# Kernel optimization log

Hardware: AMD Instinct MI355X
Metric: run time of the kernel (lower is better)

Reference implementation:

```python
import jax, jax.numpy as jnp
import numpy as np

NUM_HEADS = 16
HIDDEN = 1024
ATTN_DIM = 64            # per-head q/k dim
HEAD_OUT = 64            # per-head v dim
OUT_DIM = 1024
BATCH, SEQ = 2, 2048


def setup_inputs() -> dict:
    key = jax.random.key(0)
    ks = jax.random.split(key, 9)
    s_in = 1.0 / np.sqrt(HIDDEN)
    s_o = 1.0 / np.sqrt(NUM_HEADS * HEAD_OUT)
    return {
        "x": jax.random.normal(ks[0], (BATCH, SEQ, HIDDEN), dtype=jnp.float32),
        # Linear weights stored [in, out] so y = x @ W + b
        "Wq": jax.random.uniform(ks[1], (HIDDEN, NUM_HEADS * ATTN_DIM), jnp.float32, -s_in, s_in),
        "bq": jax.random.uniform(ks[2], (NUM_HEADS * ATTN_DIM,), jnp.float32, -s_in, s_in),
        "Wk": jax.random.uniform(ks[3], (HIDDEN, NUM_HEADS * ATTN_DIM), jnp.float32, -s_in, s_in),
        "bk": jax.random.uniform(ks[4], (NUM_HEADS * ATTN_DIM,), jnp.float32, -s_in, s_in),
        "Wv": jax.random.uniform(ks[5], (HIDDEN, NUM_HEADS * HEAD_OUT), jnp.float32, -s_in, s_in),
        "bv": jax.random.uniform(ks[6], (HIDDEN, NUM_HEADS * HEAD_OUT)[1:], jnp.float32, -s_in, s_in),
        "Wo": jax.random.uniform(ks[7], (NUM_HEADS * HEAD_OUT, OUT_DIM), jnp.float32, -s_o, s_o),
        "bo": jax.random.uniform(ks[8], (OUT_DIM,), jnp.float32, -s_o, s_o),
    }


def _split_heads(y, h):
    b, s, _ = y.shape
    return y.reshape(b, s, h, -1).transpose(0, 2, 1, 3)  # [b, h, s, d]


def reference(x, Wq, bq, Wk, bk, Wv, bv, Wo, bo):
    h = NUM_HEADS
    q = _split_heads(x @ Wq + bq, h)                    # [b,h,s,dq]
    k = _split_heads(x @ Wk + bk, h)                    # [b,h,s,dq]
    v = _split_heads(x @ Wv + bv, h)                    # [b,h,s,dv]
    scale = 1.0 / jnp.sqrt(jnp.float32(ATTN_DIM))
    # pattern[b,h,i,j] = key_i . query_j  (i=key index, j=query index)
    pattern = jnp.einsum('bhid,bhjd->bhij', k, q) * scale
    # softmax over key axis (dim=-2), matching t.softmax(..., dim=-2)
    prob = jax.nn.softmax(pattern, axis=-2)             # [b,h,key,query]
    # out[b,h,s,d] = sum_i prob[b,h,i,s] * v[b,h,i,d]
    out = jnp.einsum('bhis,bhid->bhsd', prob, v)        # [b,h,s,dv]
    b, _, s, dv = out.shape
    concat = out.transpose(0, 2, 1, 3).reshape(b, s, h * dv)
    return concat @ Wo + bo
```

## Files before the change

kernel.cpp:

```cpp
#include <hip/hip_runtime.h>
#include <cstdint>
#include <cstddef>

using f16   = _Float16;
using f16x4 = __attribute__((ext_vector_type(4))) _Float16;
using f16x8 = __attribute__((ext_vector_type(8))) _Float16;
using f32x4 = __attribute__((ext_vector_type(4))) float;

__device__ __forceinline__ f32x4 mfma16(f16x8 a, f16x8 b, f32x4 c) {
  return __builtin_amdgcn_mfma_f32_16x16x32_f16(a, b, c, 0, 0, 0);
}

__device__ __forceinline__ void gld16(const f16* g, f16* l) {
  __builtin_amdgcn_global_load_lds(
      (__attribute__((address_space(1))) void*)g,
      (__attribute__((address_space(3))) void*)l, 16, 0, 0);
}

constexpr int BATCH = 2, SEQL = 2048, HID = 1024, NH = 16, DH = 64;
constexpr int TOK = BATCH * SEQL;
constexpr int NQKV = 3 * HID;

__global__ __launch_bounds__(256) void k_convert_x(const float* __restrict__ x,
                                                   f16* __restrict__ xh) {
  int i = (blockIdx.x * 256 + threadIdx.x) * 4;
  float4 v = *(const float4*)(x + i);
  f16x4 o = { (f16)v.x, (f16)v.y, (f16)v.z, (f16)v.w };
  *(f16x4*)(xh + i) = o;
}

__global__ __launch_bounds__(256) void k_transpose(const float* __restrict__ Wq,
                                                   const float* __restrict__ Wk,
                                                   const float* __restrict__ Wv,
                                                   const float* __restrict__ Wo,
                                                   f16* __restrict__ WT,
                                                   f16* __restrict__ WoT) {
  __shared__ float tile[32][33];
  int mat = blockIdx.z;
  const float* W = (mat == 0) ? Wq : (mat == 1) ? Wk : (mat == 2) ? Wv : Wo;
  int in0 = blockIdx.x * 32, out0 = blockIdx.y * 32;
  int c = threadIdx.x & 31, r8 = threadIdx.x >> 5;
#pragma unroll
  for (int i = 0; i < 4; i++) {
    int r = r8 + i * 8;
    tile[r][c] = W[(size_t)(in0 + r) * HID + out0 + c];
  }
  __syncthreads();
#pragma unroll
  for (int i = 0; i < 4; i++) {
    int r = r8 + i * 8;
    f16 v = (f16)tile[c][r];
    if (mat == 3) WoT[(size_t)(out0 + r) * HID + in0 + c] = v;
    else          WT[(size_t)(mat * HID + out0 + r) * HID + in0 + c] = v;
  }
}

__global__ __launch_bounds__(256, 2) void k_gemm_qkv(
    const f16* __restrict__ xh, const f16* __restrict__ WT,
    const float* __restrict__ bq, const float* __restrict__ bk,
    const float* __restrict__ bv,
    f16* __restrict__ Qh, f16* __restrict__ Kh, f16* __restrict__ Vp) {
  constexpr int K = HID;
  int m0 = blockIdx.x * 128, n0 = blockIdx.y * 128;
  int tid = threadIdx.x;
  int w = tid >> 6, lane = tid & 63, lr = lane & 15, lq = lane >> 4;
  int wm = w >> 1, wn = w & 1;
  __shared__ f16 Ash[128 * 32];
  __shared__ f16 Bsh[128 * 32];
  f32x4 acc[4][4];
#pragma unroll
  for (int i = 0; i < 4; i++)
#pragma unroll
    for (int j = 0; j < 4; j++) acc[i][j] = (f32x4){0.f, 0.f, 0.f, 0.f};

  int row0 = tid >> 2, seg0 = tid & 3;
  int row1 = (256 + tid) >> 2;
  const f16* Ag0 = xh + (size_t)(m0 + row0) * K + seg0 * 8;
  const f16* Ag1 = xh + (size_t)(m0 + row1) * K + seg0 * 8;
  const f16* Bg0 = WT + (size_t)(n0 + row0) * K + seg0 * 8;
  const f16* Bg1 = WT + (size_t)(n0 + row1) * K + seg0 * 8;

  for (int k0 = 0; k0 < K; k0 += 32) {
    __syncthreads();
    gld16(Ag0 + k0, Ash + tid * 8);
    gld16(Ag1 + k0, Ash + (256 + tid) * 8);
    gld16(Bg0 + k0, Bsh + tid * 8);
    gld16(Bg1 + k0, Bsh + (256 + tid) * 8);
    __syncthreads();
    f16x8 af[4], bfr[4];
#pragma unroll
    for (int mt = 0; mt < 4; mt++)
      af[mt] = *(const f16x8*)(Ash + (wm * 64 + mt * 16 + lr) * 32 + lq * 8);
#pragma unroll
    for (int nt = 0; nt < 4; nt++)
      bfr[nt] = *(const f16x8*)(Bsh + (wn * 64 + nt * 16 + lr) * 32 + lq * 8);
#pragma unroll
    for (int mt = 0; mt < 4; mt++)
#pragma unroll
      for (int nt = 0; nt < 4; nt++)
        acc[mt][nt] = mfma16(af[mt], bfr[nt], acc[mt][nt]);
  }

#pragma unroll
  for (int nt = 0; nt < 4; nt++) {
    int o = n0 + wn * 64 + nt * 16 + lr;
    int sec = o >> 10, o1 = o & 1023, hh = o1 >> 6, dd = o1 & 63;
    float bias = (sec == 0) ? bq[o1] : (sec == 1) ? bk[o1] : bv[o1];
#pragma unroll
    for (int mt = 0; mt < 4; mt++) {
      int t0 = m0 + wm * 64 + mt * 16 + lq * 4;
      int b = t0 >> 11, s0 = t0 & (SEQL - 1);
      size_t bh = (size_t)(b * NH + hh);
      if (sec == 2) {
        f16x4 pv = { (f16)(acc[mt][nt][0] + bias), (f16)(acc[mt][nt][1] + bias),
                     (f16)(acc[mt][nt][2] + bias), (f16)(acc[mt][nt][3] + bias) };
        int pb = (s0 & ~31) | ((s0 & 12) << 1) | ((s0 >> 2) & 4);
        *(f16x4*)(Vp + (bh * DH + dd) * SEQL + pb) = pv;
      } else {
        f16* dst = (sec == 0) ? Qh : Kh;
#pragma unroll
        for (int r = 0; r < 4; r++)
          dst[(bh * SEQL + s0 + r) * DH + dd] = (f16)(acc[mt][nt][r] + bias);
      }
    }
  }
}

__global__ __launch_bounds__(512, 4) void k_attn(const f16* __restrict__ Qh,
                                                 const f16* __restrict__ Kh,
                                                 const f16* __restrict__ Vp,
                                                 f16* __restrict__ Ao) {
  int bh = blockIdx.x;
  int qblk = blockIdx.y;
  int b = bh >> 4, h = bh & 15;
  int tid = threadIdx.x;
  int w = tid >> 6;
  int g = w >> 2;
  int wq = w & 3;
  int lane = tid & 63, lr = lane & 15, lq = lane >> 4;

  __shared__ f16 sh[8 * 64 * 64];

  f16x8 qf[2][2];
#pragma unroll
  for (int qt = 0; qt < 2; qt++) {
    const f16* Qbase =
        Qh + ((size_t)bh * SEQL + qblk * 128 + wq * 32 + qt * 16 + lr) * DH;
#pragma unroll
    for (int ks = 0; ks < 2; ks++) {
      qf[qt][ks] = *(const f16x8*)(Qbase + ks * 32 + lq * 8);
      qf[qt][ks] = qf[qt][ks] * (f16)0.18033688f;
    }
  }

  f32x4 O[2][4];
#pragma unroll
  for (int qt = 0; qt < 2; qt++)
#pragma unroll
    for (int dt = 0; dt < 4; dt++) O[qt][dt] = (f32x4){0.f, 0.f, 0.f, 0.f};
  float lsum[2] = {0.f, 0.f};

  int sg = w >> 2, kv = (w >> 1) & 1, half = w & 1;
  int srow8 = lane >> 3;
  int scol = ((lane & 7) ^ srow8) * 8;
  const f16* sgl;
  size_t pstride, kbstride;
  if (kv == 0) {
    sgl = Kh + ((size_t)bh * SEQL + sg * 1024 + half * 32 + srow8) * DH + scol;
    pstride = (size_t)8 * DH;
    kbstride = (size_t)64 * DH;
  } else {
    sgl = Vp + ((size_t)bh * DH + half * 32 + srow8) * SEQL + sg * 1024 + scol;
    pstride = (size_t)8 * SEQL;
    kbstride = (size_t)64;
  }
  f16* sdst0 = sh + (sg * 4 + kv) * 4096 + half * 2048 + lane * 8;
  f16* sdst1 = sdst0 + 8192;

  int swz = lr & 7;
  int c0 = ((0 * 4 + lq) ^ swz) * 8;
  int c1 = ((1 * 4 + lq) ^ swz) * 8;

#pragma unroll
  for (int p8 = 0; p8 < 4; p8++) gld16(sgl + p8 * pstride, sdst0 + p8 * 512);

  for (int kb = 0; kb < 16; kb++) {
    __syncthreads();
    if (kb < 15) {
      const f16* src = sgl + (size_t)(kb + 1) * kbstride;
      f16* sd = ((kb + 1) & 1) ? sdst1 : sdst0;
#pragma unroll
      for (int p8 = 0; p8 < 4; p8++) gld16(src + p8 * pstride, sd + p8 * 512);
    }

    const f16* Kp = sh + (g * 4 + (kb & 1) * 2) * 4096;
    const f16* Vq = Kp + 4096;

    f32x4 sacc[2][4];
#pragma unroll
    for (int qt = 0; qt < 2; qt++)
#pragma unroll
      for (int kt = 0; kt < 4; kt++) sacc[qt][kt] = (f32x4){0.f, 0.f, 0.f, 0.f};
    __builtin_amdgcn_s_setprio(1);
#pragma unroll
    for (int ks = 0; ks < 2; ks++) {
      int kc = ks ? c1 : c0;
#pragma unroll
      for (int kt = 0; kt < 4; kt++) {
        f16x8 kf = *(const f16x8*)(Kp + (kt * 16 + lr) * 64 + kc);
        sacc[0][kt] = mfma16(kf, qf[0][ks], sacc[0][kt]);
        sacc[1][kt] = mfma16(kf, qf[1][ks], sacc[1][kt]);
      }
    }
    __builtin_amdgcn_s_setprio(0);

    f16x8 pf[2][2];
#pragma unroll
    for (int qt = 0; qt < 2; qt++) {
      float part = 0.f;
#pragma unroll
      for (int kt = 0; kt < 4; kt++) {
        float p0 = __builtin_amdgcn_exp2f(sacc[qt][kt][0]);
        float p1 = __builtin_amdgcn_exp2f(sacc[qt][kt][1]);
        float p2 = __builtin_amdgcn_exp2f(sacc[qt][kt][2]);
        float p3 = __builtin_amdgcn_exp2f(sacc[qt][kt][3]);
        part += (p0 + p1) + (p2 + p3);
        int s = kt >> 1, off = (kt & 1) * 4;
        pf[qt][s][off + 0] = (f16)p0; pf[qt][s][off + 1] = (f16)p1;
        pf[qt][s][off + 2] = (f16)p2; pf[qt][s][off + 3] = (f16)p3;
      }
      lsum[qt] += part;
    }

    __builtin_amdgcn_s_setprio(1);
#pragma unroll
    for (int s = 0; s < 2; s++) {
      int vc = s ? c1 : c0;
#pragma unroll
      for (int dt = 0; dt < 4; dt++) {
        f16x8 vf = *(const f16x8*)(Vq + (dt * 16 + lr) * 64 + vc);
        O[0][dt] = mfma16(vf, pf[0][s], O[0][dt]);
        O[1][dt] = mfma16(vf, pf[1][s], O[1][dt]);
      }
    }
    __builtin_amdgcn_s_setprio(0);
  }

  __syncthreads();
  float* part = (float*)sh;
  float* plsum = part + 128 * 64;
  if (g == 1) {
#pragma unroll
    for (int qt = 0; qt < 2; qt++) {
      int ql = wq * 32 + qt * 16 + lr;
#pragma unroll
      for (int dt = 0; dt < 4; dt++) {
        int slot = (dt * 4 + lq) ^ lr;
        *(f32x4*)(part + ql * 64 + slot * 4) = O[qt][dt];
      }
      plsum[ql * 4 + lq] = lsum[qt];
    }
  }
  __syncthreads();
  if (g == 0) {
#pragma unroll
    for (int qt = 0; qt < 2; qt++) {
      int ql = wq * 32 + qt * 16 + lr;
      float ls = lsum[qt] + plsum[ql * 4 + lq];
      float l1 = ls + __shfl_xor(ls, 16);
      float ltot = l1 + __shfl_xor(l1, 32);
      float inv = 1.0f / ltot;
      int q = qblk * 128 + ql;
      f16* dst = Ao + ((size_t)b * SEQL + q) * HID + h * DH;
#pragma unroll
      for (int dt = 0; dt < 4; dt++) {
        int slot = (dt * 4 + lq) ^ lr;
        f32x4 po = *(const f32x4*)(part + ql * 64 + slot * 4);
        f16x4 o = { (f16)((O[qt][dt][0] + po[0]) * inv),
                    (f16)((O[qt][dt][1] + po[1]) * inv),
                    (f16)((O[qt][dt][2] + po[2]) * inv),
                    (f16)((O[qt][dt][3] + po[3]) * inv) };
        *(f16x4*)(dst + dt * 16 + lq * 4) = o;
      }
    }
  }
}

__global__ __launch_bounds__(256, 2) void k_gemm_out(const f16* __restrict__ Ah,
                                                     const f16* __restrict__ WoT,
                                                     const float* __restrict__ bo,
                                                     float* __restrict__ out) {
  constexpr int K = HID;
  int m0 = blockIdx.x * 128, n0 = blockIdx.y * 64;
  int tid = threadIdx.x;
  int w = tid >> 6, lane = tid & 63, lr = lane & 15, lq = lane >> 4;
  int wm = w >> 1, wn = w & 1;
  __shared__ f16 Ash[128 * 32];
  __shared__ f16 Bsh[64 * 32];
  f32x4 acc[4][2];
#pragma unroll
  for (int i = 0; i < 4; i++)
#pragma unroll
    for (int j = 0; j < 2; j++) acc[i][j] = (f32x4){0.f, 0.f, 0.f, 0.f};

  int row0 = tid >> 2, seg0 = tid & 3;
  int row1 = (256 + tid) >> 2;
  const f16* Ag0 = Ah + (size_t)(m0 + row0) * K + seg0 * 8;
  const f16* Ag1 = Ah + (size_t)(m0 + row1) * K + seg0 * 8;
  const f16* Bg0 = WoT + (size_t)(n0 + row0) * K + seg0 * 8;

  for (int k0 = 0; k0 < K; k0 += 32) {
    __syncthreads();
    gld16(Ag0 + k0, Ash + tid * 8);
    gld16(Ag1 + k0, Ash + (256 + tid) * 8);
    gld16(Bg0 + k0, Bsh + tid * 8);
    __syncthreads();
    f16x8 af[4], bfr[2];
#pragma unroll
    for (int mt = 0; mt < 4; mt++)
      af[mt] = *(const f16x8*)(Ash + (wm * 64 + mt * 16 + lr) * 32 + lq * 8);
#pragma unroll
    for (int nt = 0; nt < 2; nt++)
      bfr[nt] = *(const f16x8*)(Bsh + (wn * 32 + nt * 16 + lr) * 32 + lq * 8);
#pragma unroll
    for (int mt = 0; mt < 4; mt++)
#pragma unroll
      for (int nt = 0; nt < 2; nt++)
        acc[mt][nt] = mfma16(af[mt], bfr[nt], acc[mt][nt]);
  }

#pragma unroll
  for (int nt = 0; nt < 2; nt++) {
    int o = n0 + wn * 32 + nt * 16 + lr;
    float bias = bo[o];
#pragma unroll
    for (int mt = 0; mt < 4; mt++) {
      int t0 = m0 + wm * 64 + mt * 16 + lq * 4;
#pragma unroll
      for (int r = 0; r < 4; r++)
        out[(size_t)(t0 + r) * HID + o] = acc[mt][nt][r] + bias;
    }
  }
}

extern "C" void kernel_launch(void* const* d_in, const int* in_sizes, int n_in,
                              void* d_out, int out_size, void* d_ws, size_t ws_size,
                              hipStream_t stream) {
  const float* x  = (const float*)d_in[0];
  const float* Wq = (const float*)d_in[1];
  const float* bq = (const float*)d_in[2];
  const float* Wk = (const float*)d_in[3];
  const float* bk = (const float*)d_in[4];
  const float* Wv = (const float*)d_in[5];
  const float* bv = (const float*)d_in[6];
  const float* Wo = (const float*)d_in[7];
  const float* bo = (const float*)d_in[8];

  char* ws = (char*)d_ws;
  f16* xh  = (f16*)(ws + 0);
  f16* WT  = (f16*)(ws + 8388608);
  f16* WoT = (f16*)(ws + 14680064);
  f16* Qh  = (f16*)(ws + 16777216);
  f16* Kh  = (f16*)(ws + 25165824);
  f16* Vp  = (f16*)(ws + 33554432);
  f16* Ao  = (f16*)(ws + 41943040);

  k_convert_x<<<TOK * HID / 1024, 256, 0, stream>>>(x, xh);
  k_transpose<<<dim3(32, 32, 4), 256, 0, stream>>>(Wq, Wk, Wv, Wo, WT, WoT);
  k_gemm_qkv<<<dim3(TOK / 128, NQKV / 128), 256, 0, stream>>>(xh, WT, bq, bk, bv,
                                                              Qh, Kh, Vp);
  k_attn<<<dim3(BATCH * NH, SEQL / 128), 512, 0, stream>>>(Qh, Kh, Vp, Ao);
  k_gemm_out<<<dim3(TOK / 128, HID / 64), 256, 0, stream>>>(Ao, WoT, bo,
                                                            (float*)d_out);
}
```

Measured before the change: 184.8 us.

## Switch attention kernel to 32x32x16 MFMA with 4 waves and fused softmax-PV

Rewrites the attention kernel to use 32x32x16 MFMA tiles instead of 16x16x32, halving the block to 256 threads with each wave owning 64 queries. Exponentials are computed per 8-key slice and fed straight into the PV MFMA, and the V permutation written by the QKV GEMM is changed to match the new fragment layout. The goal is fewer MFMA issues and fewer LDS fragment loads per unit of work; in exchange each wave carries more accumulator registers and occupancy drops.

```diff
diff --git a/kernel.cpp b/kernel.cpp
--- a/kernel.cpp
+++ b/kernel.cpp
@@ -2,13 +2,17 @@
 #include <cstdint>
 #include <cstddef>
 
-using f16   = _Float16;
-using f16x4 = __attribute__((ext_vector_type(4))) _Float16;
-using f16x8 = __attribute__((ext_vector_type(8))) _Float16;
-using f32x4 = __attribute__((ext_vector_type(4))) float;
+using f16    = _Float16;
+using f16x4  = __attribute__((ext_vector_type(4))) _Float16;
+using f16x8  = __attribute__((ext_vector_type(8))) _Float16;
+using f32x4  = __attribute__((ext_vector_type(4))) float;
+using f32x16 = __attribute__((ext_vector_type(16))) float;
 
 __device__ __forceinline__ f32x4 mfma16(f16x8 a, f16x8 b, f32x4 c) {
   return __builtin_amdgcn_mfma_f32_16x16x32_f16(a, b, c, 0, 0, 0);
+}
+__device__ __forceinline__ f32x16 mfma32(f16x8 a, f16x8 b, f32x16 c) {
+  return __builtin_amdgcn_mfma_f32_32x32x16_f16(a, b, c, 0, 0, 0);
 }
 
 __device__ __forceinline__ void gld16(const f16* g, f16* l) {
@@ -114,7 +118,7 @@
       if (sec == 2) {
         f16x4 pv = { (f16)(acc[mt][nt][0] + bias), (f16)(acc[mt][nt][1] + bias),
                      (f16)(acc[mt][nt][2] + bias), (f16)(acc[mt][nt][3] + bias) };
-        int pb = (s0 & ~31) | ((s0 & 12) << 1) | ((s0 >> 2) & 4);
+        int pb = (((s0 >> 2) ^ (s0 >> 3)) & 1) ? (s0 ^ 12) : s0;
         *(f16x4*)(Vp + (bh * DH + dd) * SEQL + pb) = pv;
       } else {
         f16* dst = (sec == 0) ? Qh : Kh;
@@ -126,7 +130,7 @@
   }
 }
 
-__global__ __launch_bounds__(512, 4) void k_attn(const f16* __restrict__ Qh,
+__global__ __launch_bounds__(256, 2) void k_attn(const f16* __restrict__ Qh,
                                                  const f16* __restrict__ Kh,
                                                  const f16* __restrict__ Vp,
                                                  f16* __restrict__ Ao) {
@@ -135,54 +139,53 @@
   int b = bh >> 4, h = bh & 15;
   int tid = threadIdx.x;
   int w = tid >> 6;
-  int g = w >> 2;
-  int wq = w & 3;
-  int lane = tid & 63, lr = lane & 15, lq = lane >> 4;
+  int g = w >> 1;
+  int wq = w & 1;
+  int lane = tid & 63;
+  int l31 = lane & 31, hh = lane >> 5, l7 = lane & 7;
 
   __shared__ f16 sh[8 * 64 * 64];
 
-  f16x8 qf[2][2];
+  f16x8 qf[2][4];
 #pragma unroll
   for (int qt = 0; qt < 2; qt++) {
     const f16* Qbase =
-        Qh + ((size_t)bh * SEQL + qblk * 128 + wq * 32 + qt * 16 + lr) * DH;
-#pragma unroll
-    for (int ks = 0; ks < 2; ks++) {
-      qf[qt][ks] = *(const f16x8*)(Qbase + ks * 32 + lq * 8);
+        Qh + ((size_t)bh * SEQL + qblk * 128 + wq * 64 + qt * 32 + l31) * DH;
+#pragma unroll
+    for (int ks = 0; ks < 4; ks++) {
+      qf[qt][ks] = *(const f16x8*)(Qbase + ks * 16 + hh * 8);
       qf[qt][ks] = qf[qt][ks] * (f16)0.18033688f;
     }
   }
 
-  f32x4 O[2][4];
-#pragma unroll
-  for (int qt = 0; qt < 2; qt++)
-#pragma unroll
-    for (int dt = 0; dt < 4; dt++) O[qt][dt] = (f32x4){0.f, 0.f, 0.f, 0.f};
+  f32x16 O[2][2];
+#pragma unroll
+  for (int dt = 0; dt < 2; dt++)
+#pragma unroll
+    for (int qt = 0; qt < 2; qt++)
+#pragma unroll
+      for (int e = 0; e < 16; e++) O[dt][qt][e] = 0.f;
   float lsum[2] = {0.f, 0.f};
 
-  int sg = w >> 2, kv = (w >> 1) & 1, half = w & 1;
+  int sg = w >> 1, kv = w & 1;
   int srow8 = lane >> 3;
   int scol = ((lane & 7) ^ srow8) * 8;
   const f16* sgl;
   size_t pstride, kbstride;
   if (kv == 0) {
-    sgl = Kh + ((size_t)bh * SEQL + sg * 1024 + half * 32 + srow8) * DH + scol;
+    sgl = Kh + ((size_t)bh * SEQL + sg * 1024 + srow8) * DH + scol;
     pstride = (size_t)8 * DH;
     kbstride = (size_t)64 * DH;
   } else {
-    sgl = Vp + ((size_t)bh * DH + half * 32 + srow8) * SEQL + sg * 1024 + scol;
+    sgl = Vp + ((size_t)bh * DH + srow8) * SEQL + sg * 1024 + scol;
     pstride = (size_t)8 * SEQL;
     kbstride = (size_t)64;
   }
-  f16* sdst0 = sh + (sg * 4 + kv) * 4096 + half * 2048 + lane * 8;
-  f16* sdst1 = sdst0 + 8192;
-
-  int swz = lr & 7;
-  int c0 = ((0 * 4 + lq) ^ swz) * 8;
-  int c1 = ((1 * 4 + lq) ^ swz) * 8;
-
-#pragma unroll
-  for (int p8 = 0; p8 < 4; p8++) gld16(sgl + p8 * pstride, sdst0 + p8 * 512);
+  f16* sdst0 = sh + ((sg * 2 + 0) * 2 + kv) * 4096 + lane * 8;
+  f16* sdst1 = sh + ((sg * 2 + 1) * 2 + kv) * 4096 + lane * 8;
+
+#pragma unroll
+  for (int p8 = 0; p8 < 8; p8++) gld16(sgl + p8 * pstride, sdst0 + p8 * 512);
 
   for (int kb = 0; kb < 16; kb++) {
     __syncthreads();
@@ -190,98 +193,101 @@
       const f16* src = sgl + (size_t)(kb + 1) * kbstride;
       f16* sd = ((kb + 1) & 1) ? sdst1 : sdst0;
 #pragma unroll
-      for (int p8 = 0; p8 < 4; p8++) gld16(src + p8 * pstride, sd + p8 * 512);
-    }
-
-    const f16* Kp = sh + (g * 4 + (kb & 1) * 2) * 4096;
+      for (int p8 = 0; p8 < 8; p8++) gld16(src + p8 * pstride, sd + p8 * 512);
+    }
+
+    const f16* Kp = sh + ((g * 2 + (kb & 1)) * 2 + 0) * 4096;
     const f16* Vq = Kp + 4096;
 
-    f32x4 sacc[2][4];
-#pragma unroll
-    for (int qt = 0; qt < 2; qt++)
-#pragma unroll
-      for (int kt = 0; kt < 4; kt++) sacc[qt][kt] = (f32x4){0.f, 0.f, 0.f, 0.f};
+    f32x16 sacc[2][2];
+#pragma unroll
+    for (int kt = 0; kt < 2; kt++)
+#pragma unroll
+      for (int qt = 0; qt < 2; qt++)
+#pragma unroll
+        for (int e = 0; e < 16; e++) sacc[kt][qt][e] = 0.f;
     __builtin_amdgcn_s_setprio(1);
 #pragma unroll
-    for (int ks = 0; ks < 2; ks++) {
-      int kc = ks ? c1 : c0;
-#pragma unroll
-      for (int kt = 0; kt < 4; kt++) {
-        f16x8 kf = *(const f16x8*)(Kp + (kt * 16 + lr) * 64 + kc);
-        sacc[0][kt] = mfma16(kf, qf[0][ks], sacc[0][kt]);
-        sacc[1][kt] = mfma16(kf, qf[1][ks], sacc[1][kt]);
+    for (int kt = 0; kt < 2; kt++) {
+#pragma unroll
+      for (int ks = 0; ks < 4; ks++) {
+        int kc = ((ks * 2 + hh) ^ l7) * 8;
+        f16x8 kf = *(const f16x8*)(Kp + (kt * 32 + l31) * 64 + kc);
+        sacc[kt][0] = mfma32(kf, qf[0][ks], sacc[kt][0]);
+        sacc[kt][1] = mfma32(kf, qf[1][ks], sacc[kt][1]);
       }
     }
     __builtin_amdgcn_s_setprio(0);
 
-    f16x8 pf[2][2];
+#pragma unroll
+    for (int kt = 0; kt < 2; kt++) {
+#pragma unroll
+      for (int s = 0; s < 2; s++) {
+        int slice = kt * 2 + s;
+        int vc = ((slice * 2 + hh) ^ l7) * 8;
+        f16x8 vf0 = *(const f16x8*)(Vq + (0 * 32 + l31) * 64 + vc);
+        f16x8 vf1 = *(const f16x8*)(Vq + (1 * 32 + l31) * 64 + vc);
+#pragma unroll
+        for (int qt = 0; qt < 2; qt++) {
+          float p0 = __builtin_amdgcn_exp2f(sacc[kt][qt][s * 8 + 0]);
+          float p1 = __builtin_amdgcn_exp2f(sacc[kt][qt][s * 8 + 1]);
+          float p2 = __builtin_amdgcn_exp2f(sacc[kt][qt][s * 8 + 2]);
+          float p3 = __builtin_amdgcn_exp2f(sacc[kt][qt][s * 8 + 3]);
+          float p4 = __builtin_amdgcn_exp2f(sacc[kt][qt][s * 8 + 4]);
+          float p5 = __builtin_amdgcn_exp2f(sacc[kt][qt][s * 8 + 5]);
+          float p6 = __builtin_amdgcn_exp2f(sacc[kt][qt][s * 8 + 6]);
+          float p7 = __builtin_amdgcn_exp2f(sacc[kt][qt][s * 8 + 7]);
+          lsum[qt] += ((p0 + p1) + (p2 + p3)) + ((p4 + p5) + (p6 + p7));
+          f16x8 pf = { (f16)p0, (f16)p1, (f16)p2, (f16)p3,
+                       (f16)p4, (f16)p5, (f16)p6, (f16)p7 };
+          O[0][qt] = mfma32(vf0, pf, O[0][qt]);
+          O[1][qt] = mfma32(vf1, pf, O[1][qt]);
+        }
+      }
+    }
+  }
+
+  __syncthreads();
+  float* mrg = (float*)sh;
+  float* pls = mrg + 128 * 64;
+  if (g == 1) {
 #pragma unroll
     for (int qt = 0; qt < 2; qt++) {
-      float part = 0.f;
-#pragma unroll
-      for (int kt = 0; kt < 4; kt++) {
-        float p0 = __builtin_amdgcn_exp2f(sacc[qt][kt][0]);
-        float p1 = __builtin_amdgcn_exp2f(sacc[qt][kt][1]);
-        float p2 = __builtin_amdgcn_exp2f(sacc[qt][kt][2]);
-        float p3 = __builtin_amdgcn_exp2f(sacc[qt][kt][3]);
-        part += (p0 + p1) + (p2 + p3);
-        int s = kt >> 1, off = (kt & 1) * 4;
-        pf[qt][s][off + 0] = (f16)p0; pf[qt][s][off + 1] = (f16)p1;
-        pf[qt][s][off + 2] = (f16)p2; pf[qt][s][off + 3] = (f16)p3;
-      }
-      lsum[qt] += part;
-    }
-
-    __builtin_amdgcn_s_setprio(1);
-#pragma unroll
-    for (int s = 0; s < 2; s++) {
-      int vc = s ? c1 : c0;
-#pragma unroll
-      for (int dt = 0; dt < 4; dt++) {
-        f16x8 vf = *(const f16x8*)(Vq + (dt * 16 + lr) * 64 + vc);
-        O[0][dt] = mfma16(vf, pf[0][s], O[0][dt]);
-        O[1][dt] = mfma16(vf, pf[1][s], O[1][dt]);
-      }
-    }
-    __builtin_amdgcn_s_setprio(0);
-  }
-
-  __syncthreads();
-  float* part = (float*)sh;
-  float* plsum = part + 128 * 64;
-  if (g == 1) {
-#pragma unroll
-    for (int qt = 0; qt < 2; qt++) {
-      int ql = wq * 32 + qt * 16 + lr;
-#pragma unroll
-      for (int dt = 0; dt < 4; dt++) {
-        int slot = (dt * 4 + lq) ^ lr;
-        *(f32x4*)(part + ql * 64 + slot * 4) = O[qt][dt];
-      }
-      plsum[ql * 4 + lq] = lsum[qt];
+      int ql = wq * 64 + qt * 32 + l31;
+#pragma unroll
+      for (int dt = 0; dt < 2; dt++)
+#pragma unroll
+        for (int j = 0; j < 4; j++) {
+          int slot = (dt * 8 + j * 2 + hh) ^ l7;
+          f32x4 v = { O[dt][qt][4 * j + 0], O[dt][qt][4 * j + 1],
+                      O[dt][qt][4 * j + 2], O[dt][qt][4 * j + 3] };
+          *(f32x4*)(mrg + ql * 64 + slot * 4) = v;
+        }
+      pls[ql * 2 + hh] = lsum[qt];
     }
   }
   __syncthreads();
   if (g == 0) {
 #pragma unroll
     for (int qt = 0; qt < 2; qt++) {
-      int ql = wq * 32 + qt * 16 + lr;
-      float ls = lsum[qt] + plsum[ql * 4 + lq];
-      float l1 = ls + __shfl_xor(ls, 16);
-      float ltot = l1 + __shfl_xor(l1, 32);
+      int ql = wq * 64 + qt * 32 + l31;
+      float ls = lsum[qt] + pls[ql * 2 + hh];
+      float ltot = ls + __shfl_xor(ls, 32);
       float inv = 1.0f / ltot;
       int q = qblk * 128 + ql;
       f16* dst = Ao + ((size_t)b * SEQL + q) * HID + h * DH;
 #pragma unroll
-      for (int dt = 0; dt < 4; dt++) {
-        int slot = (dt * 4 + lq) ^ lr;
-        f32x4 po = *(const f32x4*)(part + ql * 64 + slot * 4);
-        f16x4 o = { (f16)((O[qt][dt][0] + po[0]) * inv),
-                    (f16)((O[qt][dt][1] + po[1]) * inv),
-                    (f16)((O[qt][dt][2] + po[2]) * inv),
-                    (f16)((O[qt][dt][3] + po[3]) * inv) };
-        *(f16x4*)(dst + dt * 16 + lq * 4) = o;
-      }
+      for (int dt = 0; dt < 2; dt++)
+#pragma unroll
+        for (int j = 0; j < 4; j++) {
+          int slot = (dt * 8 + j * 2 + hh) ^ l7;
+          f32x4 po = *(const f32x4*)(mrg + ql * 64 + slot * 4);
+          f16x4 o = { (f16)((O[dt][qt][4 * j + 0] + po[0]) * inv),
+                      (f16)((O[dt][qt][4 * j + 1] + po[1]) * inv),
+                      (f16)((O[dt][qt][4 * j + 2] + po[2]) * inv),
+                      (f16)((O[dt][qt][4 * j + 3] + po[3]) * inv) };
+          *(f16x4*)(dst + dt * 32 + j * 8 + hh * 4) = o;
+        }
     }
   }
 }
@@ -369,7 +375,7 @@
   k_transpose<<<dim3(32, 32, 4), 256, 0, stream>>>(Wq, Wk, Wv, Wo, WT, WoT);
   k_gemm_qkv<<<dim3(TOK / 128, NQKV / 128), 256, 0, stream>>>(xh, WT, bq, bk, bv,
                                                               Qh, Kh, Vp);
-  k_attn<<<dim3(BATCH * NH, SEQL / 128), 512, 0, stream>>>(Qh, Kh, Vp, Ao);
+  k_attn<<<dim3(BATCH * NH, SEQL / 128), 256, 0, stream>>>(Qh, Kh, Vp, Ao);
   k_gemm_out<<<dim3(TOK / 128, HID / 64), 256, 0, stream>>>(Ao, WoT, bo,
                                                             (float*)d_out);
 }
```

Result: no change. 185.5 us (+0.4%).
